# Kernel optimization log

Measured on AMD Instinct MI355X. Metric: run time of the kernel, lower is better.

The kernel has to match this reference:

```python
import jax, jax.numpy as jnp
import numpy as np

N = 50000      # nodes
E = 600000     # edges
IN = 128       # in_channels
HID = 128      # GCN hidden width (fixed in module)
H = 4          # TransformerConv heads
C = 32         # out_channels per head (heads*C = 128)


def _lin(k, fan_in, fan_out):
    return jax.random.normal(k, (fan_in, fan_out), jnp.float32) / np.sqrt(fan_in)


def setup_inputs() -> dict:
    key = jax.random.key(0)
    ks = jax.random.split(key, 12)
    return {
        "x": jax.random.normal(ks[0], (N, IN), jnp.float32),
        "edge_index": jax.random.randint(ks[1], (2, E), 0, N, dtype=jnp.int32),
        "W_gcn": _lin(ks[2], IN, HID),
        "b_gcn": jnp.zeros((HID,), jnp.float32),
        "Wq": _lin(ks[3], HID, H * C),
        "bq": jnp.zeros((H * C,), jnp.float32),
        "Wk": _lin(ks[4], HID, H * C),
        "bk": jnp.zeros((H * C,), jnp.float32),
        "Wv": _lin(ks[5], HID, H * C),
        "bv": jnp.zeros((H * C,), jnp.float32),
        "Ws": _lin(ks[6], HID, H * C),
        "bs": jnp.zeros((H * C,), jnp.float32),
    }


def reference(x, edge_index, W_gcn, b_gcn, Wq, bq, Wk, bk, Wv, bv, Ws, bs):
    n = x.shape[0]
    idt = edge_index.dtype

    # ---- GCNConv: x' = D^{-1/2}(A+I)D^{-1/2} x W + b, then ReLU ----
    h = x @ W_gcn                                   # [N, HID] linear first (PyG order)
    loop = jnp.arange(n, dtype=idt)
    src = jnp.concatenate([edge_index[0], loop])    # with self-loops
    tgt = jnp.concatenate([edge_index[1], loop])
    deg = jax.ops.segment_sum(jnp.ones(src.shape, h.dtype), tgt, num_segments=n)
    dinv = jnp.where(deg > 0, jax.lax.rsqrt(deg), 0.0)
    norm = dinv[src] * dinv[tgt]                    # [E+N]
    h = jax.ops.segment_sum(h[src] * norm[:, None], tgt, num_segments=n)
    h = jax.nn.relu(h + b_gcn)                      # [N, HID]

    # ---- TransformerConv (heads=4, concat=True, no self-loops added) ----
    s, t = edge_index[0], edge_index[1]
    q = (h @ Wq + bq).reshape(n, H, C)
    k = (h @ Wk + bk).reshape(n, H, C)
    v = (h @ Wv + bv).reshape(n, H, C)

    alpha = jnp.einsum('ehc,ehc->eh', q[t], k[s]) / np.sqrt(C)   # [E, H]
    m = jax.lax.stop_gradient(jax.ops.segment_max(alpha, t, num_segments=n))
    ea = jnp.exp(alpha - m[t])
    denom = jax.ops.segment_sum(ea, t, num_segments=n)           # [N, H]
    w = ea / jnp.where(denom[t] > 0, denom[t], 1.0)              # softmax per target node

    out = jax.ops.segment_sum(w[:, :, None] * v[s], t, num_segments=n)  # [N, H, C]
    out = out.reshape(n, H * C)

    # root/skip connection (lin_skip)
    return out + h @ Ws + bs
```

## Files before the change

kernel.cpp:

```cpp
#include <hip/hip_runtime.h>
#include <hip/hip_bf16.h>

typedef __attribute__((ext_vector_type(8))) short short8;
typedef __attribute__((ext_vector_type(4))) float floatx4;
typedef _Float16 half2v __attribute__((ext_vector_type(2)));

__device__ __forceinline__ float ld_f(const void* p, int f32, int i) {
  if (f32) return ((const float*)p)[i];
  unsigned short u = ((const unsigned short*)p)[i];
  return __uint_as_float(((unsigned)u) << 16);
}
__device__ __forceinline__ short ld_bf(const void* p, int f32, int i) {
  if (!f32) return ((const short*)p)[i];
  __hip_bfloat16 h = __float2bfloat16(((const float*)p)[i]);
  return *reinterpret_cast<short*>(&h);
}
__device__ __forceinline__ unsigned short f_to_bfu(float v) {
  __hip_bfloat16 h = __float2bfloat16(v);
  return *reinterpret_cast<unsigned short*>(&h);
}
__device__ __forceinline__ short f_to_h(float v) {
  _Float16 h = (_Float16)v;
  return *reinterpret_cast<short*>(&h);
}
__device__ __forceinline__ float bflo(unsigned w) { return __uint_as_float(w << 16); }
__device__ __forceinline__ float bfhi(unsigned w) { return __uint_as_float(w & 0xFFFF0000u); }

__global__ void init_kernel(const unsigned short* __restrict__ xs, int* __restrict__ flag,
                            int* __restrict__ cnt, int N) {
  if (blockIdx.x == 0) {
    __shared__ int sbad;
    if (threadIdx.x == 0) sbad = 0;
    __syncthreads();
    int bad = 0;
    for (int j = 2 * threadIdx.x; j < 16384; j += 512) {
      unsigned e = (xs[j] >> 7) & 0xFF;
      if (e >= 0xF0) bad = 1;
    }
    if (bad) atomicOr(&sbad, 1);
    __syncthreads();
    if (threadIdx.x == 0) flag[0] = sbad;
    return;
  }
  int i = (blockIdx.x - 1) * blockDim.x + threadIdx.x;
  if (i < N) cnt[i] = 0;
}

__global__ void prep_hist(const void* bg, const void* bq, const void* bk, const void* bv,
                          const void* bs, const void* Wg, const void* Wq, const void* Wk,
                          const void* Wv, const void* Ws, const int* __restrict__ flag,
                          float* __restrict__ bgf, float* __restrict__ bias512,
                          short* __restrict__ WpG, short* __restrict__ WpQ,
                          const int* __restrict__ ei, int* __restrict__ cnt,
                          int* __restrict__ erank, int E, int Gp) {
  if ((int)blockIdx.x >= Gp) {
    int e = (blockIdx.x - Gp) * blockDim.x + threadIdx.x;
    if (e < E) erank[e] = atomicAdd(&cnt[ei[E + e]], 1);
    return;
  }
  int tid = blockIdx.x * blockDim.x + threadIdx.x;
  int f = *flag;
  if (tid < 128) { bgf[tid] = ld_f(bg, f, tid); return; }
  if (tid < 640) {
    int t = tid - 128;
    const void* b = (t < 128) ? bq : (t < 256) ? bk : (t < 384) ? bv : bs;
    bias512[t] = ld_f(b, f, t & 127);
    return;
  }
  if (tid < 640 + 2048) {
    int id = tid - 640;
    int lane = id & 63, kb = (id >> 6) & 3, tn = id >> 8;
    int k0 = kb * 32 + (lane >> 4) * 8;
    int n = tn * 16 + (lane & 15);
    short* dst = WpG + (size_t)id * 8;
#pragma unroll
    for (int j = 0; j < 8; ++j) dst[j] = ld_bf(Wg, f, (k0 + j) * 128 + n);
    return;
  }
  if (tid < 640 + 2048 + 8192) {
    int id = tid - 640 - 2048;
    int lane = id & 63, kb = (id >> 6) & 3, tn = id >> 8;
    int k0 = kb * 32 + (lane >> 4) * 8;
    int n = tn * 16 + (lane & 15);
    const void* W = (n < 128) ? Wq : (n < 256) ? Wk : (n < 384) ? Wv : Ws;
    int col = n & 127;
    short* dst = WpQ + (size_t)id * 8;
#pragma unroll
    for (int j = 0; j < 8; ++j) dst[j] = ld_bf(W, f, (k0 + j) * 128 + col);
  }
}

__global__ void scanA(const int* __restrict__ cnt, int* __restrict__ chunkscan,
                      int* __restrict__ partials, int N) {
  __shared__ int sh[1024];
  int t = threadIdx.x;
  int g = blockIdx.x * 1024 + t;
  int v = (g < N) ? cnt[g] : 0;
  sh[t] = v;
  __syncthreads();
  for (int o = 1; o < 1024; o <<= 1) {
    int add = (t >= o) ? sh[t - o] : 0;
    __syncthreads();
    sh[t] += add;
    __syncthreads();
  }
  if (g < N) chunkscan[g] = sh[t];
  if (t == 1023) partials[blockIdx.x] = sh[1023];
}

__global__ void scanB(int* __restrict__ partials, int nb) {
  int lane = threadIdx.x;
  if (nb <= 64) {
    int v = (lane < nb) ? partials[lane] : 0;
#pragma unroll
    for (int o = 1; o < 64; o <<= 1) {
      int t = __shfl_up(v, o);
      if (lane >= o) v += t;
    }
    int ex = __shfl_up(v, 1);
    if (lane == 0) ex = 0;
    if (lane < nb) partials[lane] = ex;
    return;
  }
  if (lane == 0) {
    int run = 0;
    for (int b = 0; b < nb; ++b) {
      int t = partials[b];
      partials[b] = run;
      run += t;
    }
  }
}

__global__ void scanC(const int* __restrict__ cnt, const int* __restrict__ chunkscan,
                      const int* __restrict__ partials, int* __restrict__ rowptr,
                      float* __restrict__ dinv, int N) {
  int g = blockIdx.x * blockDim.x + threadIdx.x;
  if (g == 0) rowptr[0] = 0;
  if (g >= N) return;
  int c = cnt[g];
  int inc = chunkscan[g] + partials[g >> 10];
  rowptr[g + 1] = inc;
  dinv[g] = rsqrtf((float)c + 1.0f);
}

__global__ void gemmh0_fill(const void* __restrict__ X, const int* __restrict__ flag,
                            const short* __restrict__ Bp, const float* __restrict__ dinv,
                            short* __restrict__ C, int M, const int* __restrict__ ei,
                            const int* __restrict__ rowptr, const int* __restrict__ erank,
                            int* __restrict__ srcs, int E, int Gg) {
  if ((int)blockIdx.x >= Gg) {
    int e = (blockIdx.x - Gg) * blockDim.x + threadIdx.x;
    if (e < E) {
      int t = ei[E + e];
      srcs[rowptr[t] + erank[e]] = ei[e];
    }
    return;
  }
  int wv = (blockIdx.x * blockDim.x + threadIdx.x) >> 6;
  int lane = threadIdx.x & 63;
  int tilesM = (M + 15) >> 4;
  if (wv >= tilesM) return;
  int f = *flag;
  int tm = wv;
  int m = tm * 16 + (lane & 15);
  int mc = m < M ? m : M - 1;
  int quad = lane >> 4;
  short8 a[4];
  if (f) {
    const float4* xr = (const float4*)((const float*)X + (size_t)mc * 128) + quad * 2;
#pragma unroll
    for (int kb = 0; kb < 4; ++kb) {
      float4 u = xr[kb * 8];
      float4 w = xr[kb * 8 + 1];
      a[kb][0] = (short)f_to_bfu(u.x);
      a[kb][1] = (short)f_to_bfu(u.y);
      a[kb][2] = (short)f_to_bfu(u.z);
      a[kb][3] = (short)f_to_bfu(u.w);
      a[kb][4] = (short)f_to_bfu(w.x);
      a[kb][5] = (short)f_to_bfu(w.y);
      a[kb][6] = (short)f_to_bfu(w.z);
      a[kb][7] = (short)f_to_bfu(w.w);
    }
  } else {
    const short* xr = (const short*)X + (size_t)mc * 128 + quad * 8;
#pragma unroll
    for (int kb = 0; kb < 4; ++kb) a[kb] = *(const short8*)(xr + kb * 32);
  }
  floatx4 acc[8];
#pragma unroll
  for (int tn = 0; tn < 8; ++tn) acc[tn] = (floatx4){0.f, 0.f, 0.f, 0.f};
#pragma unroll
  for (int kb = 0; kb < 4; ++kb) {
#pragma unroll
    for (int tn = 0; tn < 8; ++tn) {
      short8 b8 = *(const short8*)(Bp + ((size_t)(tn * 4 + kb) * 64 + lane) * 8);
      acc[tn] = __builtin_amdgcn_mfma_f32_16x16x32_bf16(a[kb], b8, acc[tn], 0, 0, 0);
    }
  }
  int row0 = tm * 16 + quad * 4;
  int cl = lane & 15;
  float dsc[4];
#pragma unroll
  for (int r = 0; r < 4; ++r) dsc[r] = (row0 + r < M) ? dinv[row0 + r] : 0.f;
#pragma unroll
  for (int tn = 0; tn < 8; ++tn)
#pragma unroll
    for (int r = 0; r < 4; ++r)
      if (row0 + r < M)
        C[(size_t)(row0 + r) * 128 + tn * 16 + cl] = (short)f_to_bfu(acc[tn][r] * dsc[r]);
}

__global__ __launch_bounds__(512) void gather_qkvs(
    const int* __restrict__ rowptr, const int* __restrict__ srcs,
    const float* __restrict__ dinv, const unsigned* __restrict__ h0,
    const float* __restrict__ bgf, const short* __restrict__ Bp,
    const float* __restrict__ bias512, short* __restrict__ qb,
    short* __restrict__ kvb, short* __restrict__ skipb, int N) {
  __shared__ short hsm[16][136];
  int tileBase = blockIdx.x * 16;
  int wv = threadIdx.x >> 6;
  int lane = threadIdx.x & 63;
  int hf = lane >> 5, q2 = (lane >> 4) & 1, sl = lane & 15, sl32 = lane & 31;
  int node = tileBase + wv * 2 + hf;
  int nodec = node < N ? node : N - 1;
  int beg = rowptr[nodec], end = rowptr[nodec + 1];
  int deg = node < N ? end - beg : 0;
  int dm1 = deg - 1;
  int dmc = dm1 > 0 ? dm1 : 0;
  int sreg = srcs[deg > 0 ? beg + (sl32 < dm1 ? sl32 : dm1) : 0];
  int degmax = deg;
  degmax = max(degmax, __shfl_xor(degmax, 32));
  int dd = degmax < 32 ? degmax : 32;
  int hb = hf << 5;
  float a0 = 0.f, a1 = 0.f, a2 = 0.f, a3 = 0.f, a4 = 0.f, a5 = 0.f, a6 = 0.f, a7 = 0.f;
  for (int base = 0; base < dd; base += 8) {
    int p0 = base + q2, p1 = p0 + 2, p2 = p0 + 4, p3 = p0 + 6;
    int s0 = __shfl(sreg, hb + (p0 < dmc ? p0 : dmc));
    int s1 = __shfl(sreg, hb + (p1 < dmc ? p1 : dmc));
    int s2 = __shfl(sreg, hb + (p2 < dmc ? p2 : dmc));
    int s3 = __shfl(sreg, hb + (p3 < dmc ? p3 : dmc));
    float m0 = p0 < deg ? 1.f : 0.f;
    float m1 = p1 < deg ? 1.f : 0.f;
    float m2 = p2 < deg ? 1.f : 0.f;
    float m3 = p3 < deg ? 1.f : 0.f;
    uint4 w0 = *(const uint4*)(h0 + (size_t)s0 * 64 + sl * 4);
    uint4 w1 = *(const uint4*)(h0 + (size_t)s1 * 64 + sl * 4);
    uint4 w2 = *(const uint4*)(h0 + (size_t)s2 * 64 + sl * 4);
    uint4 w3 = *(const uint4*)(h0 + (size_t)s3 * 64 + sl * 4);
    a0 += m0 * bflo(w0.x) + m1 * bflo(w1.x) + m2 * bflo(w2.x) + m3 * bflo(w3.x);
    a1 += m0 * bfhi(w0.x) + m1 * bfhi(w1.x) + m2 * bfhi(w2.x) + m3 * bfhi(w3.x);
    a2 += m0 * bflo(w0.y) + m1 * bflo(w1.y) + m2 * bflo(w2.y) + m3 * bflo(w3.y);
    a3 += m0 * bfhi(w0.y) + m1 * bfhi(w1.y) + m2 * bfhi(w2.y) + m3 * bfhi(w3.y);
    a4 += m0 * bflo(w0.z) + m1 * bflo(w1.z) + m2 * bflo(w2.z) + m3 * bflo(w3.z);
    a5 += m0 * bfhi(w0.z) + m1 * bfhi(w1.z) + m2 * bfhi(w2.z) + m3 * bfhi(w3.z);
    a6 += m0 * bflo(w0.w) + m1 * bflo(w1.w) + m2 * bflo(w2.w) + m3 * bflo(w3.w);
    a7 += m0 * bfhi(w0.w) + m1 * bfhi(w1.w) + m2 * bfhi(w2.w) + m3 * bfhi(w3.w);
  }
  for (int i = beg + 32 + q2; i < end; i += 2) {
    uint4 w0 = *(const uint4*)(h0 + (size_t)srcs[i] * 64 + sl * 4);
    a0 += bflo(w0.x);
    a1 += bfhi(w0.x);
    a2 += bflo(w0.y);
    a3 += bfhi(w0.y);
    a4 += bflo(w0.z);
    a5 += bfhi(w0.z);
    a6 += bflo(w0.w);
    a7 += bfhi(w0.w);
  }
  a0 += __shfl_xor(a0, 16);
  a1 += __shfl_xor(a1, 16);
  a2 += __shfl_xor(a2, 16);
  a3 += __shfl_xor(a3, 16);
  a4 += __shfl_xor(a4, 16);
  a5 += __shfl_xor(a5, 16);
  a6 += __shfl_xor(a6, 16);
  a7 += __shfl_xor(a7, 16);
  if (q2 == 0) {
    uint4 hw = *(const uint4*)(h0 + (size_t)nodec * 64 + sl * 4);
    float dt = dinv[nodec];
    const float4* bb = (const float4*)bgf;
    float4 b0 = bb[sl * 2], b1 = bb[sl * 2 + 1];
    float v0 = (a0 + bflo(hw.x)) * dt + b0.x;
    float v1 = (a1 + bfhi(hw.x)) * dt + b0.y;
    float v2 = (a2 + bflo(hw.y)) * dt + b0.z;
    float v3 = (a3 + bfhi(hw.y)) * dt + b0.w;
    float v4 = (a4 + bflo(hw.z)) * dt + b1.x;
    float v5 = (a5 + bfhi(hw.z)) * dt + b1.y;
    float v6 = (a6 + bflo(hw.w)) * dt + b1.z;
    float v7 = (a7 + bfhi(hw.w)) * dt + b1.w;
    v0 = v0 > 0.f ? v0 : 0.f;
    v1 = v1 > 0.f ? v1 : 0.f;
    v2 = v2 > 0.f ? v2 : 0.f;
    v3 = v3 > 0.f ? v3 : 0.f;
    v4 = v4 > 0.f ? v4 : 0.f;
    v5 = v5 > 0.f ? v5 : 0.f;
    v6 = v6 > 0.f ? v6 : 0.f;
    v7 = v7 > 0.f ? v7 : 0.f;
    uint4 o;
    o.x = (unsigned)f_to_bfu(v0) | ((unsigned)f_to_bfu(v1) << 16);
    o.y = (unsigned)f_to_bfu(v2) | ((unsigned)f_to_bfu(v3) << 16);
    o.z = (unsigned)f_to_bfu(v4) | ((unsigned)f_to_bfu(v5) << 16);
    o.w = (unsigned)f_to_bfu(v6) | ((unsigned)f_to_bfu(v7) << 16);
    *(uint4*)(&hsm[wv * 2 + hf][sl * 8]) = o;
  }
  __syncthreads();
  int mrow = lane & 15;
  int quad = lane >> 4;
  short8 a[4];
#pragma unroll
  for (int kb = 0; kb < 4; ++kb)
    a[kb] = *(const short8*)(&hsm[mrow][quad * 8 + kb * 32]);
  floatx4 acc[4];
#pragma unroll
  for (int j = 0; j < 4; ++j) acc[j] = (floatx4){0.f, 0.f, 0.f, 0.f};
#pragma unroll
  for (int kb = 0; kb < 4; ++kb) {
#pragma unroll
    for (int j = 0; j < 4; ++j) {
      int tn = wv * 4 + j;
      short8 b8 = *(const short8*)(Bp + ((size_t)(tn * 4 + kb) * 64 + lane) * 8);
      acc[j] = __builtin_amdgcn_mfma_f32_16x16x32_bf16(a[kb], b8, acc[j], 0, 0, 0);
    }
  }
  int row0 = tileBase + quad * 4;
  int cl = lane & 15;
  int tng = wv >> 1;
#pragma unroll
  for (int j = 0; j < 4; ++j) {
    int cc = ((wv & 1) * 4 + j) * 16 + cl;
    float b = bias512[tng * 128 + cc];
#pragma unroll
    for (int r = 0; r < 4; ++r) {
      int row = row0 + r;
      if (row >= N) continue;
      float val = acc[j][r] + b;
      if (tng == 0) {
        qb[(size_t)row * 128 + cc] = f_to_h(val);
      } else if (tng == 3) {
        skipb[(size_t)row * 128 + cc] = (short)f_to_bfu(val);
      } else {
        size_t base = (size_t)row * 256 + (size_t)((cc >> 2) * 8 + (cc & 3));
        if (tng == 1)
          kvb[base] = f_to_h(val);
        else
          kvb[base + 4] = (short)f_to_bfu(val);
      }
    }
  }
}

__device__ __forceinline__ float dpp_red8(float p) {
  p += __int_as_float(__builtin_amdgcn_mov_dpp(__float_as_int(p), 0xB1, 0xF, 0xF, true));
  p += __int_as_float(__builtin_amdgcn_mov_dpp(__float_as_int(p), 0x4E, 0xF, 0xF, true));
  p += __int_as_float(__builtin_amdgcn_mov_dpp(__float_as_int(p), 0x141, 0xF, 0xF, true));
  return p;
}
__device__ __forceinline__ float dot_dpp(half2v qa, half2v qc, unsigned kw0, unsigned kw1) {
  half2v k0 = *reinterpret_cast<half2v*>(&kw0);
  half2v k1 = *reinterpret_cast<half2v*>(&kw1);
#if __has_builtin(__builtin_amdgcn_fdot2)
  float p = __builtin_amdgcn_fdot2(qa, k0, 0.f, false);
  p = __builtin_amdgcn_fdot2(qc, k1, p, false);
#else
  float p = (float)qa[0] * (float)k0[0] + (float)qa[1] * (float)k0[1] +
            (float)qc[0] * (float)k1[0] + (float)qc[1] * (float)k1[1];
#endif
  return dpp_red8(p) * 0.17677669529663687f;
}

__global__ void attn_fused(const int* __restrict__ rowptr, const int* __restrict__ srcs,
                           const unsigned* __restrict__ qb, const unsigned* __restrict__ kvb,
                           const unsigned* __restrict__ skipb, float* __restrict__ out, int N) {
  int node = (int)((blockIdx.x * (long long)blockDim.x + threadIdx.x) >> 6);
  if (node >= N) return;
  int lane = threadIdx.x & 63;
  int hf = lane >> 5, sl = lane & 31;
  uint2 qw = *(const uint2*)(qb + (size_t)node * 64 + sl * 2);
  half2v qa = *reinterpret_cast<half2v*>(&qw.x);
  half2v qc = *reinterpret_cast<half2v*>(&qw.y);
  int beg = rowptr[node], end = rowptr[node + 1];
  int deg = end - beg;
  int dm1 = deg - 1;
  int dmc = dm1 > 0 ? dm1 : 0;
  int sreg = srcs[deg > 0 ? beg + (lane < dm1 ? lane : dm1) : 0];
  int dd = deg < 64 ? deg : 64;

  float denom = 0.f, ax0 = 0.f, ax1 = 0.f, ax2 = 0.f, ax3 = 0.f;
  for (int base = 0; base < dd; base += 16) {
    uint4 kv[8];
    int pp[8];
#pragma unroll
    for (int j = 0; j < 8; ++j) {
      int p = base + hf + 2 * j;
      pp[j] = p;
      int s = __shfl(sreg, p < dmc ? p : dmc);
      kv[j] = *(const uint4*)(kvb + (size_t)s * 128 + sl * 4);
    }
#pragma unroll
    for (int j = 0; j < 8; ++j) {
      float e = __expf(dot_dpp(qa, qc, kv[j].x, kv[j].y));
      e = pp[j] < deg ? e : 0.f;
      denom += e;
      ax0 += e * bflo(kv[j].z);
      ax1 += e * bfhi(kv[j].z);
      ax2 += e * bflo(kv[j].w);
      ax3 += e * bfhi(kv[j].w);
    }
  }
  for (int i = beg + 64 + hf; i < end; i += 2) {
    int s0 = srcs[i];
    uint4 kv0 = *(const uint4*)(kvb + (size_t)s0 * 128 + sl * 4);
    float e0 = __expf(dot_dpp(qa, qc, kv0.x, kv0.y));
    denom += e0;
    ax0 += e0 * bflo(kv0.z);
    ax1 += e0 * bfhi(kv0.z);
    ax2 += e0 * bflo(kv0.w);
    ax3 += e0 * bfhi(kv0.w);
  }
  denom += __shfl_xor(denom, 32);
  ax0 += __shfl_xor(ax0, 32);
  ax1 += __shfl_xor(ax1, 32);
  ax2 += __shfl_xor(ax2, 32);
  ax3 += __shfl_xor(ax3, 32);
  if (hf == 0) {
    float r = denom > 0.f ? 1.f / denom : 0.f;
    uint2 sw = *(const uint2*)(skipb + (size_t)node * 64 + sl * 2);
    float4 o;
    o.x = ax0 * r + bflo(sw.x);
    o.y = ax1 * r + bfhi(sw.x);
    o.z = ax2 * r + bflo(sw.y);
    o.w = ax3 * r + bfhi(sw.y);
    *(float4*)(out + (size_t)node * 128 + sl * 4) = o;
  }
}

extern "C" void kernel_launch(void* const* d_in, const int* in_sizes, int n_in,
                              void* d_out, int out_size, void* d_ws, size_t ws_size,
                              hipStream_t stream) {
  const void* x  = d_in[0];
  const int* ei  = (const int*)d_in[1];
  const void* Wg = d_in[2];
  const void* bg = d_in[3];
  const void* Wq = d_in[4];
  const void* bq = d_in[5];
  const void* Wk = d_in[6];
  const void* bk = d_in[7];
  const void* Wv = d_in[8];
  const void* bv = d_in[9];
  const void* Ws = d_in[10];
  const void* bs = d_in[11];
  float* out = (float*)d_out;

  const int N = in_sizes[0] / 128;
  const int E = in_sizes[1] / 2;
  int tilesM = (N + 15) / 16;
  int nscan = (N + 1023) / 1024;
  const int B = 256;

  char* ws = (char*)d_ws;
  size_t off = 0;
  auto carve = [&](size_t bytes) -> void* {
    void* p = ws + off;
    off += (bytes + 255) & ~(size_t)255;
    return p;
  };
  int* flag = (int*)carve(256);
  float* bias512 = (float*)carve(512 * 4);
  float* bgf = (float*)carve(128 * 4);
  float* dinv = (float*)carve((size_t)N * 4);
  int* cnt = (int*)carve((size_t)N * 4);
  int* rowptr = (int*)carve((size_t)(N + 1) * 4);
  int* chunkscan = (int*)carve((size_t)N * 4);
  int* partials = (int*)carve((size_t)(nscan + 1) * 4);
  int* srcs = (int*)carve((size_t)E * 4);
  int* erank = (int*)carve((size_t)E * 4);
  short* WpG = (short*)carve((size_t)16384 * 2);
  short* WpQ = (short*)carve((size_t)65536 * 2);
  short* h0bf = (short*)carve((size_t)N * 128 * 2);
  short* qb = (short*)carve((size_t)N * 128 * 2);
  short* kvb = (short*)carve((size_t)N * 256 * 2);
  short* skipb = (short*)carve((size_t)N * 128 * 2);

  int Gp = (10880 + B - 1) / B;
  int Gh = (E + B - 1) / B;
  int Gg = (tilesM * 64 + B - 1) / B;
  int Gf = (E + B - 1) / B;

  init_kernel<<<1 + (N + B - 1) / B, B, 0, stream>>>((const unsigned short*)x, flag, cnt, N);
  prep_hist<<<Gp + Gh, B, 0, stream>>>(bg, bq, bk, bv, bs, Wg, Wq, Wk, Wv, Ws, flag,
                                       bgf, bias512, WpG, WpQ, ei, cnt, erank, E, Gp);
  scanA<<<nscan, 1024, 0, stream>>>(cnt, chunkscan, partials, N);
  scanB<<<1, 64, 0, stream>>>(partials, nscan);
  scanC<<<(N + B - 1) / B, B, 0, stream>>>(cnt, chunkscan, partials, rowptr, dinv, N);
  gemmh0_fill<<<Gg + Gf, B, 0, stream>>>(x, flag, WpG, dinv, h0bf, N, ei, rowptr, erank,
                                         srcs, E, Gg);
  gather_qkvs<<<tilesM, 512, 0, stream>>>(rowptr, srcs, dinv, (const unsigned*)h0bf, bgf,
                                          WpQ, bias512, qb, kvb, skipb, N);
  attn_fused<<<(N + 3) / 4, B, 0, stream>>>(rowptr, srcs, (const unsigned*)qb,
                                            (const unsigned*)kvb, (const unsigned*)skipb, out, N);
}
```

Baseline: 246.3 us.

## Gather one node per 16-lane quarter-wave and process 32-node tiles per block

The GCN gather in gather_qkvs now assigns one node to each 16-lane group, so a wave covers four nodes instead of two. This removes the cross-half shuffle reduction and lets every lane write to shared memory. Each block now handles 32 nodes and runs the MFMA projection twice, so the B-fragment loads are reused across two row tiles and the grid is half as large. The trade-off is less memory-level parallelism per node: each node's neighbours are walked serially in steps of four rather than split across two lane groups. The block count also drops, which lowers occupancy.

```diff
diff --git a/kernel.cpp b/kernel.cpp
--- a/kernel.cpp
+++ b/kernel.cpp
@@ -217,33 +217,37 @@
     const float* __restrict__ bgf, const short* __restrict__ Bp,
     const float* __restrict__ bias512, short* __restrict__ qb,
     short* __restrict__ kvb, short* __restrict__ skipb, int N) {
-  __shared__ short hsm[16][136];
-  int tileBase = blockIdx.x * 16;
+  __shared__ short hsm[32][136];
+  int tileBase = blockIdx.x * 32;
   int wv = threadIdx.x >> 6;
   int lane = threadIdx.x & 63;
-  int hf = lane >> 5, q2 = (lane >> 4) & 1, sl = lane & 15, sl32 = lane & 31;
-  int node = tileBase + wv * 2 + hf;
+  int q = lane >> 4, sl = lane & 15;
+  int qb16 = q << 4;
+  int node = tileBase + wv * 4 + q;
   int nodec = node < N ? node : N - 1;
   int beg = rowptr[nodec], end = rowptr[nodec + 1];
   int deg = node < N ? end - beg : 0;
   int dm1 = deg - 1;
   int dmc = dm1 > 0 ? dm1 : 0;
-  int sreg = srcs[deg > 0 ? beg + (sl32 < dm1 ? sl32 : dm1) : 0];
+  int sb = deg > 0 ? beg : 0;
+  int sreg0 = srcs[sb + (sl < dmc ? sl : dmc)];
+  int sreg1 = srcs[sb + (16 + sl < dmc ? 16 + sl : dmc)];
   int degmax = deg;
+  degmax = max(degmax, __shfl_xor(degmax, 16));
   degmax = max(degmax, __shfl_xor(degmax, 32));
   int dd = degmax < 32 ? degmax : 32;
-  int hb = hf << 5;
   float a0 = 0.f, a1 = 0.f, a2 = 0.f, a3 = 0.f, a4 = 0.f, a5 = 0.f, a6 = 0.f, a7 = 0.f;
-  for (int base = 0; base < dd; base += 8) {
-    int p0 = base + q2, p1 = p0 + 2, p2 = p0 + 4, p3 = p0 + 6;
-    int s0 = __shfl(sreg, hb + (p0 < dmc ? p0 : dmc));
-    int s1 = __shfl(sreg, hb + (p1 < dmc ? p1 : dmc));
-    int s2 = __shfl(sreg, hb + (p2 < dmc ? p2 : dmc));
-    int s3 = __shfl(sreg, hb + (p3 < dmc ? p3 : dmc));
-    float m0 = p0 < deg ? 1.f : 0.f;
-    float m1 = p1 < deg ? 1.f : 0.f;
-    float m2 = p2 < deg ? 1.f : 0.f;
-    float m3 = p3 < deg ? 1.f : 0.f;
+  for (int base = 0; base < dd; base += 4) {
+    int srs = (base & 16) ? sreg1 : sreg0;
+    int i0 = qb16 + (base & 15);
+    int s0 = __shfl(srs, i0);
+    int s1 = __shfl(srs, i0 + 1);
+    int s2 = __shfl(srs, i0 + 2);
+    int s3 = __shfl(srs, i0 + 3);
+    float m0 = base + 0 < deg ? 1.f : 0.f;
+    float m1 = base + 1 < deg ? 1.f : 0.f;
+    float m2 = base + 2 < deg ? 1.f : 0.f;
+    float m3 = base + 3 < deg ? 1.f : 0.f;
     uint4 w0 = *(const uint4*)(h0 + (size_t)s0 * 64 + sl * 4);
     uint4 w1 = *(const uint4*)(h0 + (size_t)s1 * 64 + sl * 4);
     uint4 w2 = *(const uint4*)(h0 + (size_t)s2 * 64 + sl * 4);
@@ -257,7 +261,7 @@
     a6 += m0 * bflo(w0.w) + m1 * bflo(w1.w) + m2 * bflo(w2.w) + m3 * bflo(w3.w);
     a7 += m0 * bfhi(w0.w) + m1 * bfhi(w1.w) + m2 * bfhi(w2.w) + m3 * bfhi(w3.w);
   }
-  for (int i = beg + 32 + q2; i < end; i += 2) {
+  for (int i = beg + 32; i < end; ++i) {
     uint4 w0 = *(const uint4*)(h0 + (size_t)srcs[i] * 64 + sl * 4);
     a0 += bflo(w0.x);
     a1 += bfhi(w0.x);
@@ -268,15 +272,7 @@
     a6 += bflo(w0.w);
     a7 += bfhi(w0.w);
   }
-  a0 += __shfl_xor(a0, 16);
-  a1 += __shfl_xor(a1, 16);
-  a2 += __shfl_xor(a2, 16);
-  a3 += __shfl_xor(a3, 16);
-  a4 += __shfl_xor(a4, 16);
-  a5 += __shfl_xor(a5, 16);
-  a6 += __shfl_xor(a6, 16);
-  a7 += __shfl_xor(a7, 16);
-  if (q2 == 0) {
+  {
     uint4 hw = *(const uint4*)(h0 + (size_t)nodec * 64 + sl * 4);
     float dt = dinv[nodec];
     const float4* bb = (const float4*)bgf;
@@ -302,49 +298,52 @@
     o.y = (unsigned)f_to_bfu(v2) | ((unsigned)f_to_bfu(v3) << 16);
     o.z = (unsigned)f_to_bfu(v4) | ((unsigned)f_to_bfu(v5) << 16);
     o.w = (unsigned)f_to_bfu(v6) | ((unsigned)f_to_bfu(v7) << 16);
-    *(uint4*)(&hsm[wv * 2 + hf][sl * 8]) = o;
+    *(uint4*)(&hsm[wv * 4 + q][sl * 8]) = o;
   }
   __syncthreads();
   int mrow = lane & 15;
   int quad = lane >> 4;
-  short8 a[4];
-#pragma unroll
-  for (int kb = 0; kb < 4; ++kb)
-    a[kb] = *(const short8*)(&hsm[mrow][quad * 8 + kb * 32]);
-  floatx4 acc[4];
-#pragma unroll
-  for (int j = 0; j < 4; ++j) acc[j] = (floatx4){0.f, 0.f, 0.f, 0.f};
-#pragma unroll
-  for (int kb = 0; kb < 4; ++kb) {
-#pragma unroll
-    for (int j = 0; j < 4; ++j) {
-      int tn = wv * 4 + j;
-      short8 b8 = *(const short8*)(Bp + ((size_t)(tn * 4 + kb) * 64 + lane) * 8);
-      acc[j] = __builtin_amdgcn_mfma_f32_16x16x32_bf16(a[kb], b8, acc[j], 0, 0, 0);
-    }
-  }
-  int row0 = tileBase + quad * 4;
   int cl = lane & 15;
   int tng = wv >> 1;
 #pragma unroll
-  for (int j = 0; j < 4; ++j) {
-    int cc = ((wv & 1) * 4 + j) * 16 + cl;
-    float b = bias512[tng * 128 + cc];
-#pragma unroll
-    for (int r = 0; r < 4; ++r) {
-      int row = row0 + r;
-      if (row >= N) continue;
-      float val = acc[j][r] + b;
-      if (tng == 0) {
-        qb[(size_t)row * 128 + cc] = f_to_h(val);
-      } else if (tng == 3) {
-        skipb[(size_t)row * 128 + cc] = (short)f_to_bfu(val);
-      } else {
-        size_t base = (size_t)row * 256 + (size_t)((cc >> 2) * 8 + (cc & 3));
-        if (tng == 1)
-          kvb[base] = f_to_h(val);
-        else
-          kvb[base + 4] = (short)f_to_bfu(val);
+  for (int t = 0; t < 2; ++t) {
+    short8 a[4];
+#pragma unroll
+    for (int kb = 0; kb < 4; ++kb)
+      a[kb] = *(const short8*)(&hsm[t * 16 + mrow][quad * 8 + kb * 32]);
+    floatx4 acc[4];
+#pragma unroll
+    for (int j = 0; j < 4; ++j) acc[j] = (floatx4){0.f, 0.f, 0.f, 0.f};
+#pragma unroll
+    for (int kb = 0; kb < 4; ++kb) {
+#pragma unroll
+      for (int j = 0; j < 4; ++j) {
+        int tn = wv * 4 + j;
+        short8 b8 = *(const short8*)(Bp + ((size_t)(tn * 4 + kb) * 64 + lane) * 8);
+        acc[j] = __builtin_amdgcn_mfma_f32_16x16x32_bf16(a[kb], b8, acc[j], 0, 0, 0);
+      }
+    }
+    int row0 = tileBase + t * 16 + quad * 4;
+#pragma unroll
+    for (int j = 0; j < 4; ++j) {
+      int cc = ((wv & 1) * 4 + j) * 16 + cl;
+      float b = bias512[tng * 128 + cc];
+#pragma unroll
+      for (int r = 0; r < 4; ++r) {
+        int row = row0 + r;
+        if (row >= N) continue;
+        float val = acc[j][r] + b;
+        if (tng == 0) {
+          qb[(size_t)row * 128 + cc] = f_to_h(val);
+        } else if (tng == 3) {
+          skipb[(size_t)row * 128 + cc] = (short)f_to_bfu(val);
+        } else {
+          size_t base = (size_t)row * 256 + (size_t)((cc >> 2) * 8 + (cc & 3));
+          if (tng == 1)
+            kvb[base] = f_to_h(val);
+          else
+            kvb[base + 4] = (short)f_to_bfu(val);
+        }
       }
     }
   }
@@ -495,8 +494,8 @@
   scanC<<<(N + B - 1) / B, B, 0, stream>>>(cnt, chunkscan, partials, rowptr, dinv, N);
   gemmh0_fill<<<Gg + Gf, B, 0, stream>>>(x, flag, WpG, dinv, h0bf, N, ei, rowptr, erank,
                                          srcs, E, Gg);
-  gather_qkvs<<<tilesM, 512, 0, stream>>>(rowptr, srcs, dinv, (const unsigned*)h0bf, bgf,
-                                          WpQ, bias512, qb, kvb, skipb, N);
+  gather_qkvs<<<(N + 31) / 32, 512, 0, stream>>>(rowptr, srcs, dinv, (const unsigned*)h0bf,
+                                                 bgf, WpQ, bias512, qb, kvb, skipb, N);
   attn_fused<<<(N + 3) / 4, B, 0, stream>>>(rowptr, srcs, (const unsigned*)qb,
                                             (const unsigned*)kvb, (const unsigned*)skipb, out, N);
 }
```

Result: slower. 252.8 us (+2.7%).
